# Optimization experiments

Measured on AMD Instinct MI355X. Metric: run time of the kernel, lower is better.

The kernel has to match this reference:

```python
import jax, jax.numpy as jnp
import numpy as np

B, S, H = 4, 2048, 1024
DECAY_RATE = 0.5  # MemoryModule decay: exp(-decay_rate * k), k=1 (most recent pattern)


def setup_inputs() -> dict:
    key = jax.random.key(0)
    ks = jax.random.split(key, 7)
    hidden_states = jax.random.normal(ks[0], (B, S, H), dtype=jnp.float32)
    # past attention pattern: valid row-stochastic attention probs [B, S, S]
    pa = jax.random.uniform(ks[1], (B, S, S), dtype=jnp.float32)
    past_attention = pa / pa.sum(-1, keepdims=True)
    scale = 1.0 / np.sqrt(H).astype(np.float32)
    Wq = jax.random.normal(ks[2], (H, H), dtype=jnp.float32) * scale
    Wk = jax.random.normal(ks[3], (H, H), dtype=jnp.float32) * scale
    Wv = jax.random.normal(ks[4], (H, H), dtype=jnp.float32) * scale
    Wm = jax.random.normal(ks[5], (H, H), dtype=jnp.float32) * scale
    w_gate = jax.random.normal(ks[6], (H,), dtype=jnp.float32) * scale
    return {"hidden_states": hidden_states, "past_attention": past_attention,
            "Wq": Wq, "Wk": Wk, "Wv": Wv, "Wm": Wm, "w_gate": w_gate}


def reference(hidden_states, past_attention, Wq, Wk, Wv, Wm, w_gate):
    h = hidden_states.shape[-1]
    inv_sqrt_h = 1.0 / (h ** 0.5)
    # QKV projections (hidden -> hidden)
    q = jnp.einsum('bsh,hd->bsd', hidden_states, Wq)
    k = jnp.einsum('bsh,hd->bsd', hidden_states, Wk)
    v = jnp.einsum('bsh,hd->bsd', hidden_states, Wv)
    # base attention scores QK^T / sqrt(H)
    scores = jnp.einsum('bqd,bkd->bqk', q, k) * inv_sqrt_h
    # --- memory bias ---
    # decayed history pattern (single most-recent entry, k=1)
    memory = past_attention * jnp.exp(jnp.float32(-DECAY_RATE * 1.0))  # [B,S,S]
    # per-token scalar gate from query
    gates = jax.nn.sigmoid(jnp.einsum('bsh,h->bs', q, w_gate))  # [B,S]
    memory_values = jnp.einsum('bqk,bkd->bqd', memory, v)        # memory @ V
    transformed = jnp.einsum('bsh,hd->bsd', memory_values, Wm)   # memory_transform (no bias)
    gated_memory = gates[..., None] * transformed
    memory_bias = jnp.einsum('bqd,bkd->bqk', gated_memory, k) * inv_sqrt_h
    # augmented attention
    probs = jax.nn.softmax(scores + memory_bias, axis=-1)
    context = jnp.einsum('bqk,bkd->bqd', probs, v)
    return context
```

## Files before the change

kernel.cpp:

```cpp
#include <hip/hip_runtime.h>
#include <hip/hip_bf16.h>

typedef __attribute__((ext_vector_type(4))) float f32x4;
typedef __attribute__((ext_vector_type(8))) __bf16 bf16x8;

__device__ __forceinline__ unsigned short f2bf(float f) {
    union { float f; unsigned u; } x; x.f = f;
    unsigned r = x.u + 0x7fffu + ((x.u >> 16) & 1u);
    return (unsigned short)(r >> 16);
}
__device__ __forceinline__ float bf2f(unsigned short b) {
    union { unsigned u; float f; } x; x.u = ((unsigned)b) << 16;
    return x.f;
}

__device__ __forceinline__ void gload16(const void* g, void* l) {
    __builtin_amdgcn_global_load_lds(
        (const __attribute__((address_space(1))) unsigned int*)g,
        (__attribute__((address_space(3))) unsigned int*)l,
        16, 0, 0);
}

template <int N> __device__ __forceinline__ void vm_wait();
template <> __device__ __forceinline__ void vm_wait<0>() { asm volatile("s_waitcnt vmcnt(0)" ::: "memory"); }
template <> __device__ __forceinline__ void vm_wait<2>() { asm volatile("s_waitcnt vmcnt(2)" ::: "memory"); }
template <> __device__ __forceinline__ void vm_wait<4>() { asm volatile("s_waitcnt vmcnt(4)" ::: "memory"); }

__global__ void k_convert_scale(const float* __restrict__ in, unsigned short* __restrict__ out,
                                int n4, float scale) {
    int i = blockIdx.x * 256 + threadIdx.x;
    if (i >= n4) return;
    float4 v = reinterpret_cast<const float4*>(in)[i];
    union { unsigned short u[4]; uint2 q; } o;
    o.u[0] = f2bf(v.x * scale);
    o.u[1] = f2bf(v.y * scale);
    o.u[2] = f2bf(v.z * scale);
    o.u[3] = f2bf(v.w * scale);
    reinterpret_cast<uint2*>(out)[i] = o.q;
}

__global__ void k_transpose_w(const float* __restrict__ W0, const float* __restrict__ W1,
                              const float* __restrict__ W2, const float* __restrict__ W3,
                              unsigned short* __restrict__ out) {
    __shared__ float tile[32][33];
    const float* src = blockIdx.z == 0 ? W0 : blockIdx.z == 1 ? W1 : blockIdx.z == 2 ? W2 : W3;
    unsigned short* dst = out + (size_t)blockIdx.z * 1024 * 1024;
    int lx = threadIdx.x & 31, ly8 = threadIdx.x >> 5;
    int x = blockIdx.x * 32 + lx;
#pragma unroll
    for (int i = 0; i < 4; i++) {
        int ly = ly8 + i * 8;
        tile[ly][lx] = src[(size_t)(blockIdx.y * 32 + ly) * 1024 + x];
    }
    __syncthreads();
    int tx = blockIdx.y * 32 + lx;
#pragma unroll
    for (int i = 0; i < 4; i++) {
        int ty = ly8 + i * 8;
        dst[(size_t)(blockIdx.x * 32 + ty) * 1024 + tx] = f2bf(tile[lx][ty]);
    }
}

__global__ void k_transpose_v(const unsigned short* __restrict__ C3, unsigned short* __restrict__ out) {
    __shared__ unsigned short tile[32][33];
    int bz = blockIdx.z;
    int lx = threadIdx.x & 31, ly8 = threadIdx.x >> 5;
    int x = blockIdx.x * 32 + lx;
#pragma unroll
    for (int i = 0; i < 4; i++) {
        int y = blockIdx.y * 32 + ly8 + i * 8;
        tile[ly8 + i * 8][lx] = C3[(size_t)(bz * 2048 + y) * 3072 + 2048 + x];
    }
    __syncthreads();
    int tx = blockIdx.y * 32 + lx;
#pragma unroll
    for (int i = 0; i < 4; i++) {
        int ty = blockIdx.x * 32 + ly8 + i * 8;
        out[(size_t)bz * 1024 * 2048 + (size_t)ty * 2048 + tx] = tile[lx][ly8 + i * 8];
    }
}

__global__ void k_rowdot(const float* __restrict__ A, const float* __restrict__ x,
                         float* __restrict__ out, int ncols, int sig) {
    int lane = threadIdx.x & 63;
    int row = blockIdx.x * 4 + (threadIdx.x >> 6);
    const float4* a = reinterpret_cast<const float4*>(A + (size_t)row * ncols);
    const float4* xv = reinterpret_cast<const float4*>(x);
    float s = 0.f;
    int n4 = ncols >> 2;
    for (int i = lane; i < n4; i += 64) {
        float4 av = a[i], bv = xv[i];
        s += av.x * bv.x + av.y * bv.y + av.z * bv.z + av.w * bv.w;
    }
#pragma unroll
    for (int o = 1; o < 64; o <<= 1) s += __shfl_xor(s, o);
    if (lane == 0) out[row] = sig ? (1.f / (1.f + __expf(-s))) : s;
}

__global__ __launch_bounds__(256) void k_softmax(const float* __restrict__ logits,
                                                 unsigned short* __restrict__ probs) {
    __shared__ float red[8];
    size_t base = (size_t)blockIdx.x * 2048;
    const float4* src = reinterpret_cast<const float4*>(logits + base);
    int t = threadIdx.x;
    int wave = t >> 6, lane = t & 63;
    float4 v0 = src[t], v1 = src[t + 256];
    float m = fmaxf(fmaxf(fmaxf(v0.x, v0.y), fmaxf(v0.z, v0.w)),
                    fmaxf(fmaxf(v1.x, v1.y), fmaxf(v1.z, v1.w)));
#pragma unroll
    for (int o = 1; o < 64; o <<= 1) m = fmaxf(m, __shfl_xor(m, o));
    if (lane == 0) red[wave] = m;
    __syncthreads();
    m = fmaxf(fmaxf(red[0], red[1]), fmaxf(red[2], red[3]));
    float e[8];
    e[0] = __expf(v0.x - m); e[1] = __expf(v0.y - m);
    e[2] = __expf(v0.z - m); e[3] = __expf(v0.w - m);
    e[4] = __expf(v1.x - m); e[5] = __expf(v1.y - m);
    e[6] = __expf(v1.z - m); e[7] = __expf(v1.w - m);
    float s = e[0] + e[1] + e[2] + e[3] + e[4] + e[5] + e[6] + e[7];
#pragma unroll
    for (int o = 1; o < 64; o <<= 1) s += __shfl_xor(s, o);
    if (lane == 0) red[4 + wave] = s;
    __syncthreads();
    s = red[4] + red[5] + red[6] + red[7];
    float inv = 1.f / s;
    union { unsigned short u[4]; uint2 q; } o0, o1;
#pragma unroll
    for (int j = 0; j < 4; j++) o0.u[j] = f2bf(e[j] * inv);
#pragma unroll
    for (int j = 0; j < 4; j++) o1.u[j] = f2bf(e[4 + j] * inv);
    reinterpret_cast<uint2*>(probs + base)[t] = o0.q;
    reinterpret_cast<uint2*>(probs + base)[t + 256] = o1.q;
}

template <int BN>
struct Geo {
    static constexpr int WN = BN / 64;
    static constexpr int WM = 8 / WN;
    static constexpr int WROWS = 256 / WM;
    static constexpr int MF = WROWS / 16;
    static constexpr int MP = MF / 4;
    static constexpr int ASZ = 256 * 64 * 2;
    static constexpr int BSZ = BN * 64 * 2;
    static constexpr int BUFSZ = ASZ + BSZ;
};

#define GPH(BUFOFF, MB, LB, STG, VMW)                                                   \
    {                                                                                   \
        const char* aB = smem + (BUFOFF);                                               \
        const char* bB = aB + G::ASZ;                                                   \
        bf16x8 af[G::MP * 2];                                                           \
        _Pragma("unroll") for (int mm = 0; mm < G::MP; ++mm)                            \
        _Pragma("unroll") for (int kk = 0; kk < 2; ++kk) {                              \
            int rowx = wrow + ((MB) + mm) * 16 + fr;                                    \
            int slot = (kk * 4 + kq) ^ (rowx & 7);                                      \
            af[mm * 2 + kk] = *reinterpret_cast<const bf16x8*>(aB + rowx * 128 + slot * 16); \
        }                                                                               \
        if (LB) {                                                                       \
            _Pragma("unroll") for (int nn = 0; nn < 4; ++nn)                            \
            _Pragma("unroll") for (int kk = 0; kk < 2; ++kk) {                          \
                int rowx = wcol + nn * 16 + fr;                                         \
                int slot = (kk * 4 + kq) ^ (rowx & 7);                                  \
                bfrag[nn * 2 + kk] = *reinterpret_cast<const bf16x8*>(bB + rowx * 128 + slot * 16); \
            }                                                                           \
        }                                                                               \
        STG;                                                                            \
        __builtin_amdgcn_sched_barrier(0);                                              \
        VMW;                                                                            \
        __builtin_amdgcn_s_barrier();                                                   \
        asm volatile("s_waitcnt lgkmcnt(0)" ::: "memory");                              \
        __builtin_amdgcn_sched_barrier(0);                                              \
        __builtin_amdgcn_s_setprio(1);                                                  \
        _Pragma("unroll") for (int mm = 0; mm < G::MP; ++mm)                            \
        _Pragma("unroll") for (int nn = 0; nn < 4; ++nn)                                \
        _Pragma("unroll") for (int kk = 0; kk < 2; ++kk)                                \
            acc[(MB) + mm][nn] = __builtin_amdgcn_mfma_f32_16x16x32_bf16(               \
                af[mm * 2 + kk], bfrag[nn * 2 + kk], acc[(MB) + mm][nn], 0, 0, 0);      \
        __builtin_amdgcn_s_setprio(0);                                                  \
        __builtin_amdgcn_sched_barrier(0);                                              \
        __builtin_amdgcn_s_barrier();                                                   \
        __builtin_amdgcn_sched_barrier(0);                                              \
    }

template <int EPI, int BN>
__global__ __launch_bounds__(512, 2) void k_gemm8(
    const unsigned short* __restrict__ A, int ldA, long long bsA,
    const unsigned short* __restrict__ Bt, int ldB, long long bsB,
    void* __restrict__ Cv, int ldC, long long bsC,
    const unsigned short* __restrict__ Qm, int ldQ,
    const float* __restrict__ gates, float alpha, int K, int NX, int NY) {
    using G = Geo<BN>;
    extern __shared__ char smem[];
    const int NT = K >> 6, NI = K >> 7;

    unsigned b = blockIdx.x;
    unsigned wg = (b & 7) * (gridDim.x >> 3) + (b >> 3);
    int xT = wg % NX;
    unsigned r2 = wg / NX;
    int yT = r2 % NY;
    int zB = r2 / NY;

    const unsigned short* Ab = A + (size_t)zB * (size_t)bsA;
    const unsigned short* Bb = Bt + (size_t)zB * (size_t)bsB;

    int t = threadIdx.x, lane = t & 63, wave = t >> 6;
    int wc = wave % G::WN, wr = wave / G::WN;
    int fr = lane & 15, kq = lane >> 4;
    int wrow = wr * G::WROWS, wcol = wc * 64;
    int trow = t >> 3, csx = (t & 7) ^ (trow & 7);
    long long rowTile = (long long)yT * 256, colTile = (long long)xT * BN;

    f32x4 acc[G::MF][4];
#pragma unroll
    for (int m = 0; m < G::MF; ++m)
#pragma unroll
        for (int n = 0; n < 4; ++n) acc[m][n] = (f32x4){0.f, 0.f, 0.f, 0.f};
    bf16x8 bfrag[8];

    auto stageA = [&](int buf, int h, int tt) {
        int kt = tt < NT ? tt : NT - 1;
#pragma unroll
        for (int rr = 0; rr < 2; ++rr) {
            const unsigned short* src =
                Ab + (size_t)(rowTile + h * 128 + rr * 64 + trow) * (size_t)ldA + kt * 64 + csx * 8;
            gload16(src, smem + buf * G::BUFSZ + h * 16384 + rr * 8192 + t * 16);
        }
    };
    auto stageB = [&](int buf, int h, int tt) {
        int kt = tt < NT ? tt : NT - 1;
        if (BN == 256) {
#pragma unroll
            for (int rr = 0; rr < 2; ++rr) {
                const unsigned short* src =
                    Bb + (size_t)(colTile + h * 128 + rr * 64 + trow) * (size_t)ldB + kt * 64 + csx * 8;
                gload16(src, smem + buf * G::BUFSZ + G::ASZ + h * 16384 + rr * 8192 + t * 16);
            }
        } else {
            const unsigned short* src =
                Bb + (size_t)(colTile + h * 64 + trow) * (size_t)ldB + kt * 64 + csx * 8;
            gload16(src, smem + buf * G::BUFSZ + G::ASZ + h * 8192 + t * 16);
        }
    };

    stageA(0, 0, 0); stageA(0, 1, 0);
    stageB(0, 0, 0); stageB(0, 1, 0);
    stageB(1, 0, 1); stageB(1, 1, 1);
    __builtin_amdgcn_sched_barrier(0);
    vm_wait<0>();
    __builtin_amdgcn_s_barrier();
    __builtin_amdgcn_sched_barrier(0);

    constexpr int VMN = (BN == 256) ? 4 : 2;
    for (int i = 0; i < NI; ++i) {
        int t1 = 2 * i + 1, t2 = 2 * i + 2, t3 = 2 * i + 3;
        GPH(0,          0,         1, stageA(1, 0, t1), (void)0);
        GPH(0,          G::MP,     0, stageA(1, 1, t1), (void)0);
        GPH(0,          2 * G::MP, 0, stageB(0, 0, t2), (void)0);
        GPH(0,          3 * G::MP, 0, stageB(0, 1, t2), vm_wait<VMN>());
        GPH(G::BUFSZ,   0,         1, stageA(0, 0, t2), (void)0);
        GPH(G::BUFSZ,   G::MP,     0, stageA(0, 1, t2), (void)0);
        GPH(G::BUFSZ,   2 * G::MP, 0, stageB(1, 0, t3), (void)0);
        GPH(G::BUFSZ,   3 * G::MP, 0, stageB(1, 1, t3), vm_wait<VMN>());
    }
    vm_wait<0>();

    long long rb0 = rowTile + wrow + kq * 4;
    long long cb0 = colTile + wcol + fr;
    if (EPI == 0) {
        unsigned short* C = (unsigned short*)Cv + (size_t)zB * (size_t)bsC;
#pragma unroll
        for (int m = 0; m < G::MF; ++m)
#pragma unroll
            for (int n = 0; n < 4; ++n)
#pragma unroll
                for (int r = 0; r < 4; ++r)
                    C[(size_t)(rb0 + m * 16 + r) * (size_t)ldC + cb0 + n * 16] =
                        f2bf(acc[m][n][r] * alpha);
    } else if (EPI == 1) {
        unsigned short* C = (unsigned short*)Cv;
#pragma unroll
        for (int m = 0; m < G::MF; ++m)
#pragma unroll
            for (int r = 0; r < 4; ++r) {
                long long row = rb0 + m * 16 + r;
                float g = gates[row];
#pragma unroll
                for (int n = 0; n < 4; ++n) {
                    long long col = cb0 + n * 16;
                    float v = (bf2f(Qm[(size_t)row * (size_t)ldQ + col]) + g * acc[m][n][r]) * alpha;
                    C[(size_t)row * (size_t)ldC + col] = f2bf(v);
                }
            }
    } else {
        float* C = (float*)Cv + (size_t)zB * (size_t)bsC;
#pragma unroll
        for (int m = 0; m < G::MF; ++m)
#pragma unroll
            for (int n = 0; n < 4; ++n)
#pragma unroll
                for (int r = 0; r < 4; ++r)
                    C[(size_t)(rb0 + m * 16 + r) * (size_t)ldC + cb0 + n * 16] =
                        acc[m][n][r] * alpha;
    }
}

extern "C" void kernel_launch(void* const* d_in, const int* in_sizes, int n_in,
                              void* d_out, int out_size, void* d_ws, size_t ws_size,
                              hipStream_t stream) {
    const float* hs = (const float*)d_in[0];
    const float* pa = (const float*)d_in[1];
    const float* Wq = (const float*)d_in[2];
    const float* Wk = (const float*)d_in[3];
    const float* Wv = (const float*)d_in[4];
    const float* Wm = (const float*)d_in[5];
    const float* wg = (const float*)d_in[6];
    float* out = (float*)d_out;

    const int B = 4, S = 2048, H = 1024;
    const size_t BS = (size_t)B * S;
    const size_t BSH = BS * H;
    const size_t BSS = (size_t)B * S * S;
    const float inv_sqrt_h = 0.03125f;
    const float decay = 0.60653065971263342f;

    char* ws = (char*)d_ws;
    size_t off = 0;
    auto take = [&](size_t bytes) {
        char* p = ws + off;
        off += (bytes + 255) & ~(size_t)255;
        return p;
    };
    unsigned short* hs_bf = (unsigned short*)take(BSH * 2);
    unsigned short* WT    = (unsigned short*)take(4ull * H * H * 2);
    float* wg2            = (float*)take(H * 4);
    float* gates          = (float*)take(BS * 4);
    unsigned short* C3    = (unsigned short*)take(BS * 3 * H * 2);
    unsigned short* v_t   = (unsigned short*)take(BSH * 2);
    unsigned short* pa_bf = (unsigned short*)take(BSS * 2);
    float* logits         = (float*)take(BSS * 4);
    unsigned short* mv    = (unsigned short*)d_out;
    unsigned short* u_bf  = hs_bf;
    unsigned short* probs = pa_bf;
    unsigned short* WmT   = WT + 3ull * H * H;

    (void)hipFuncSetAttribute((const void*)k_gemm8<0, 128>, hipFuncAttributeMaxDynamicSharedMemorySize, 98304);
    (void)hipFuncSetAttribute((const void*)k_gemm8<1, 128>, hipFuncAttributeMaxDynamicSharedMemorySize, 98304);
    (void)hipFuncSetAttribute((const void*)k_gemm8<2, 128>, hipFuncAttributeMaxDynamicSharedMemorySize, 98304);
    (void)hipFuncSetAttribute((const void*)k_gemm8<2, 256>, hipFuncAttributeMaxDynamicSharedMemorySize, 131072);

    k_convert_scale<<<dim3((unsigned)(BSH / 4 / 256)), 256, 0, stream>>>(hs, hs_bf, (int)(BSH / 4), 1.0f);
    k_convert_scale<<<dim3((unsigned)(BSS / 4 / 256)), 256, 0, stream>>>(pa, pa_bf, (int)(BSS / 4), decay);
    k_transpose_w<<<dim3(32, 32, 4), 256, 0, stream>>>(Wq, Wk, Wv, Wm, WT);
    k_rowdot<<<dim3(H / 4), 256, 0, stream>>>(Wq, wg, wg2, H, 0);
    k_rowdot<<<dim3((unsigned)(BS / 4)), 256, 0, stream>>>(hs, wg2, gates, H, 1);

    k_gemm8<0, 128><<<768, 512, 98304, stream>>>(
        hs_bf, H, 0, WT, H, 0, C3, 3 * H, 0, nullptr, 0, nullptr, 1.f, H, 24, 32);
    k_transpose_v<<<dim3(32, 64, 4), 256, 0, stream>>>(C3, v_t);
    k_gemm8<0, 128><<<256, 512, 98304, stream>>>(
        pa_bf, S, (long long)S * S, v_t, S, (long long)H * S, mv, H, (long long)S * H,
        nullptr, 0, nullptr, 1.f, S, 8, 8);
    k_gemm8<1, 128><<<256, 512, 98304, stream>>>(
        mv, H, 0, WmT, H, 0, u_bf, H, 0, C3, 3 * H, gates, inv_sqrt_h, H, 8, 32);
    k_gemm8<2, 256><<<256, 512, 131072, stream>>>(
        u_bf, H, (long long)S * H, C3 + H, 3 * H, (long long)S * 3 * H,
        logits, S, (long long)S * S, nullptr, 0, nullptr, 1.f, H, 8, 8);
    k_softmax<<<dim3((unsigned)BS), 256, 0, stream>>>(logits, probs);
    k_gemm8<2, 128><<<256, 512, 98304, stream>>>(
        probs, S, (long long)S * S, v_t, S, (long long)H * S, out, H, (long long)S * H,
        nullptr, 0, nullptr, 1.f, S, 8, 8);
}
```

Baseline: 274.9 us.

## Use split-K with 256-wide tiles for the S-length GEMMs, plus a reduction pass

The two K=S batched GEMMs (memory@V and probs@V) now use BN=256 tiles with a split-K of 2. Each writes fp32 partial sums into the logits scratch, and a new elementwise kernel adds the two partials and converts to bf16 or fp32. The QKV projection moves to 256-wide tiles with half the blocks. The goal is larger tiles with more data reuse while keeping 256 blocks in the grid. The cost is extra fp32 partial traffic, two additional kernel launches, and a changed fp32 summation order.

```diff
diff --git a/kernel.cpp b/kernel.cpp
--- a/kernel.cpp
+++ b/kernel.cpp
@@ -37,6 +37,30 @@
     o.u[2] = f2bf(v.z * scale);
     o.u[3] = f2bf(v.w * scale);
     reinterpret_cast<uint2*>(out)[i] = o.q;
+}
+
+__global__ void k_reduce2_bf(const float* __restrict__ p0, const float* __restrict__ p1,
+                             unsigned short* __restrict__ out, int n4) {
+    int i = blockIdx.x * 256 + threadIdx.x;
+    if (i >= n4) return;
+    float4 a = reinterpret_cast<const float4*>(p0)[i];
+    float4 b = reinterpret_cast<const float4*>(p1)[i];
+    union { unsigned short u[4]; uint2 q; } o;
+    o.u[0] = f2bf(a.x + b.x);
+    o.u[1] = f2bf(a.y + b.y);
+    o.u[2] = f2bf(a.z + b.z);
+    o.u[3] = f2bf(a.w + b.w);
+    reinterpret_cast<uint2*>(out)[i] = o.q;
+}
+__global__ void k_reduce2_f32(const float* __restrict__ p0, const float* __restrict__ p1,
+                              float* __restrict__ out, int n4) {
+    int i = blockIdx.x * 256 + threadIdx.x;
+    if (i >= n4) return;
+    float4 a = reinterpret_cast<const float4*>(p0)[i];
+    float4 b = reinterpret_cast<const float4*>(p1)[i];
+    float4 o;
+    o.x = a.x + b.x; o.y = a.y + b.y; o.z = a.z + b.z; o.w = a.w + b.w;
+    reinterpret_cast<float4*>(out)[i] = o;
 }
 
 __global__ void k_transpose_w(const float* __restrict__ W0, const float* __restrict__ W1,
@@ -188,7 +212,8 @@
     const unsigned short* __restrict__ Bt, int ldB, long long bsB,
     void* __restrict__ Cv, int ldC, long long bsC,
     const unsigned short* __restrict__ Qm, int ldQ,
-    const float* __restrict__ gates, float alpha, int K, int NX, int NY) {
+    const float* __restrict__ gates, float alpha, int K,
+    int NX, int NY, int NB, int NC) {
     using G = Geo<BN>;
     extern __shared__ char smem[];
     const int NT = K >> 6, NI = K >> 7;
@@ -198,10 +223,13 @@
     int xT = wg % NX;
     unsigned r2 = wg / NX;
     int yT = r2 % NY;
-    int zB = r2 / NY;
-
-    const unsigned short* Ab = A + (size_t)zB * (size_t)bsA;
-    const unsigned short* Bb = Bt + (size_t)zB * (size_t)bsB;
+    unsigned r3 = r2 / NY;
+    int zB = r3 % NB;
+    int c = r3 / NB;
+    int zC = c * NB + zB;
+
+    const unsigned short* Ab = A + (size_t)zB * (size_t)bsA + (size_t)c * (size_t)K;
+    const unsigned short* Bb = Bt + (size_t)zB * (size_t)bsB + (size_t)c * (size_t)K;
 
     int t = threadIdx.x, lane = t & 63, wave = t >> 6;
     int wc = wave % G::WN, wr = wave / G::WN;
@@ -267,7 +295,7 @@
     long long rb0 = rowTile + wrow + kq * 4;
     long long cb0 = colTile + wcol + fr;
     if (EPI == 0) {
-        unsigned short* C = (unsigned short*)Cv + (size_t)zB * (size_t)bsC;
+        unsigned short* C = (unsigned short*)Cv + (size_t)zC * (size_t)bsC;
 #pragma unroll
         for (int m = 0; m < G::MF; ++m)
 #pragma unroll
@@ -292,7 +320,7 @@
                 }
             }
     } else {
-        float* C = (float*)Cv + (size_t)zB * (size_t)bsC;
+        float* C = (float*)Cv + (size_t)zC * (size_t)bsC;
 #pragma unroll
         for (int m = 0; m < G::MF; ++m)
 #pragma unroll
@@ -342,10 +370,11 @@
     unsigned short* u_bf  = hs_bf;
     unsigned short* probs = pa_bf;
     unsigned short* WmT   = WT + 3ull * H * H;
-
-    (void)hipFuncSetAttribute((const void*)k_gemm8<0, 128>, hipFuncAttributeMaxDynamicSharedMemorySize, 98304);
+    float* part0 = logits;
+    float* part1 = logits + BSH;
+
+    (void)hipFuncSetAttribute((const void*)k_gemm8<0, 256>, hipFuncAttributeMaxDynamicSharedMemorySize, 131072);
     (void)hipFuncSetAttribute((const void*)k_gemm8<1, 128>, hipFuncAttributeMaxDynamicSharedMemorySize, 98304);
-    (void)hipFuncSetAttribute((const void*)k_gemm8<2, 128>, hipFuncAttributeMaxDynamicSharedMemorySize, 98304);
     (void)hipFuncSetAttribute((const void*)k_gemm8<2, 256>, hipFuncAttributeMaxDynamicSharedMemorySize, 131072);
 
     k_convert_scale<<<dim3((unsigned)(BSH / 4 / 256)), 256, 0, stream>>>(hs, hs_bf, (int)(BSH / 4), 1.0f);
@@ -354,19 +383,21 @@
     k_rowdot<<<dim3(H / 4), 256, 0, stream>>>(Wq, wg, wg2, H, 0);
     k_rowdot<<<dim3((unsigned)(BS / 4)), 256, 0, stream>>>(hs, wg2, gates, H, 1);
 
-    k_gemm8<0, 128><<<768, 512, 98304, stream>>>(
-        hs_bf, H, 0, WT, H, 0, C3, 3 * H, 0, nullptr, 0, nullptr, 1.f, H, 24, 32);
+    k_gemm8<0, 256><<<384, 512, 131072, stream>>>(
+        hs_bf, H, 0, WT, H, 0, C3, 3 * H, 0, nullptr, 0, nullptr, 1.f, H, 12, 32, 1, 1);
     k_transpose_v<<<dim3(32, 64, 4), 256, 0, stream>>>(C3, v_t);
-    k_gemm8<0, 128><<<256, 512, 98304, stream>>>(
-        pa_bf, S, (long long)S * S, v_t, S, (long long)H * S, mv, H, (long long)S * H,
-        nullptr, 0, nullptr, 1.f, S, 8, 8);
+    k_gemm8<2, 256><<<256, 512, 131072, stream>>>(
+        pa_bf, S, (long long)S * S, v_t, S, (long long)H * S, part0, H, (long long)S * H,
+        nullptr, 0, nullptr, 1.f, S / 2, 4, 8, 4, 2);
+    k_reduce2_bf<<<dim3((unsigned)(BSH / 4 / 256)), 256, 0, stream>>>(part0, part1, mv, (int)(BSH / 4));
     k_gemm8<1, 128><<<256, 512, 98304, stream>>>(
-        mv, H, 0, WmT, H, 0, u_bf, H, 0, C3, 3 * H, gates, inv_sqrt_h, H, 8, 32);
+        mv, H, 0, WmT, H, 0, u_bf, H, 0, C3, 3 * H, gates, inv_sqrt_h, H, 8, 32, 1, 1);
     k_gemm8<2, 256><<<256, 512, 131072, stream>>>(
         u_bf, H, (long long)S * H, C3 + H, 3 * H, (long long)S * 3 * H,
-        logits, S, (long long)S * S, nullptr, 0, nullptr, 1.f, H, 8, 8);
+        logits, S, (long long)S * S, nullptr, 0, nullptr, 1.f, H, 8, 8, 4, 1);
     k_softmax<<<dim3((unsigned)BS), 256, 0, stream>>>(logits, probs);
-    k_gemm8<2, 128><<<256, 512, 98304, stream>>>(
-        probs, S, (long long)S * S, v_t, S, (long long)H * S, out, H, (long long)S * H,
-        nullptr, 0, nullptr, 1.f, S, 8, 8);
-}
+    k_gemm8<2, 256><<<256, 512, 131072, stream>>>(
+        probs, S, (long long)S * S, v_t, S, (long long)H * S, part0, H, (long long)S * H,
+        nullptr, 0, nullptr, 1.f, S / 2, 4, 8, 4, 2);
+    k_reduce2_f32<<<dim3((unsigned)(BSH / 4 / 256)), 256, 0, stream>>>(part0, part1, out, (int)(BSH / 4));
+}
```

Result: slower. 304.8 us (+10.9%).

## Fuse prep and post kernels, compute gates from bf16 Q, reorder GEMM tile mapping

Applied to the files above, without the earlier changes.

Merges the conversion of hidden states, the conversion of past attention and the weight transposes into one launch. It also merges the V transpose with the gate computation, which now dots the bf16 Q already held in C3 with w_gate instead of precomputing Wq·w_gate and a separate fp32 row-dot over hidden states. It further adds a y-fastest block-to-tile mapping option for the batched GEMMs to improve L2 reuse of the B operand. This cuts launch count and removes a pass over fp32 hidden states, at the cost of slightly lower gate precision because Q is bf16.

```diff
diff --git a/kernel.cpp b/kernel.cpp
--- a/kernel.cpp
+++ b/kernel.cpp
@@ -26,75 +26,89 @@
 template <> __device__ __forceinline__ void vm_wait<2>() { asm volatile("s_waitcnt vmcnt(2)" ::: "memory"); }
 template <> __device__ __forceinline__ void vm_wait<4>() { asm volatile("s_waitcnt vmcnt(4)" ::: "memory"); }
 
-__global__ void k_convert_scale(const float* __restrict__ in, unsigned short* __restrict__ out,
-                                int n4, float scale) {
-    int i = blockIdx.x * 256 + threadIdx.x;
-    if (i >= n4) return;
-    float4 v = reinterpret_cast<const float4*>(in)[i];
-    union { unsigned short u[4]; uint2 q; } o;
-    o.u[0] = f2bf(v.x * scale);
-    o.u[1] = f2bf(v.y * scale);
-    o.u[2] = f2bf(v.z * scale);
-    o.u[3] = f2bf(v.w * scale);
-    reinterpret_cast<uint2*>(out)[i] = o.q;
-}
-
-__global__ void k_transpose_w(const float* __restrict__ W0, const float* __restrict__ W1,
-                              const float* __restrict__ W2, const float* __restrict__ W3,
-                              unsigned short* __restrict__ out) {
+__global__ __launch_bounds__(256) void k_prep(
+    const float* __restrict__ hs, const float* __restrict__ pa,
+    const float* __restrict__ Wq, const float* __restrict__ Wk,
+    const float* __restrict__ Wv, const float* __restrict__ Wm,
+    unsigned short* __restrict__ hs_bf, unsigned short* __restrict__ pa_bf,
+    unsigned short* __restrict__ WT, float decay) {
     __shared__ float tile[32][33];
-    const float* src = blockIdx.z == 0 ? W0 : blockIdx.z == 1 ? W1 : blockIdx.z == 2 ? W2 : W3;
-    unsigned short* dst = out + (size_t)blockIdx.z * 1024 * 1024;
-    int lx = threadIdx.x & 31, ly8 = threadIdx.x >> 5;
-    int x = blockIdx.x * 32 + lx;
-#pragma unroll
-    for (int i = 0; i < 4; i++) {
-        int ly = ly8 + i * 8;
-        tile[ly][lx] = src[(size_t)(blockIdx.y * 32 + ly) * 1024 + x];
-    }
-    __syncthreads();
-    int tx = blockIdx.y * 32 + lx;
-#pragma unroll
-    for (int i = 0; i < 4; i++) {
-        int ty = ly8 + i * 8;
-        dst[(size_t)(blockIdx.x * 32 + ty) * 1024 + tx] = f2bf(tile[lx][ty]);
-    }
-}
-
-__global__ void k_transpose_v(const unsigned short* __restrict__ C3, unsigned short* __restrict__ out) {
+    unsigned b = blockIdx.x;
+    int t = threadIdx.x;
+    if (b < 16384u) {
+        int i = b * 256 + t;
+        float4 v = reinterpret_cast<const float4*>(pa)[i];
+        union { unsigned short u[4]; uint2 q; } o;
+        o.u[0] = f2bf(v.x * decay); o.u[1] = f2bf(v.y * decay);
+        o.u[2] = f2bf(v.z * decay); o.u[3] = f2bf(v.w * decay);
+        reinterpret_cast<uint2*>(pa_bf)[i] = o.q;
+    } else if (b < 24576u) {
+        int i = (b - 16384u) * 256 + t;
+        float4 v = reinterpret_cast<const float4*>(hs)[i];
+        union { unsigned short u[4]; uint2 q; } o;
+        o.u[0] = f2bf(v.x); o.u[1] = f2bf(v.y);
+        o.u[2] = f2bf(v.z); o.u[3] = f2bf(v.w);
+        reinterpret_cast<uint2*>(hs_bf)[i] = o.q;
+    } else {
+        unsigned bb = b - 24576u;
+        int z = bb >> 10, rem = bb & 1023;
+        int bx = rem & 31, by = rem >> 5;
+        const float* src = z == 0 ? Wq : z == 1 ? Wk : z == 2 ? Wv : Wm;
+        unsigned short* dst = WT + (size_t)z * 1024 * 1024;
+        int lx = t & 31, ly8 = t >> 5;
+        int x = bx * 32 + lx;
+#pragma unroll
+        for (int i = 0; i < 4; i++)
+            tile[ly8 + i * 8][lx] = src[(size_t)(by * 32 + ly8 + i * 8) * 1024 + x];
+        __syncthreads();
+        int tx = by * 32 + lx;
+#pragma unroll
+        for (int i = 0; i < 4; i++)
+            dst[(size_t)(bx * 32 + ly8 + i * 8) * 1024 + tx] = f2bf(tile[lx][ly8 + i * 8]);
+    }
+}
+
+__global__ __launch_bounds__(256) void k_post(
+    const unsigned short* __restrict__ C3, unsigned short* __restrict__ v_t,
+    const float* __restrict__ wg, float* __restrict__ gates) {
     __shared__ unsigned short tile[32][33];
-    int bz = blockIdx.z;
-    int lx = threadIdx.x & 31, ly8 = threadIdx.x >> 5;
-    int x = blockIdx.x * 32 + lx;
-#pragma unroll
-    for (int i = 0; i < 4; i++) {
-        int y = blockIdx.y * 32 + ly8 + i * 8;
-        tile[ly8 + i * 8][lx] = C3[(size_t)(bz * 2048 + y) * 3072 + 2048 + x];
-    }
-    __syncthreads();
-    int tx = blockIdx.y * 32 + lx;
-#pragma unroll
-    for (int i = 0; i < 4; i++) {
-        int ty = blockIdx.x * 32 + ly8 + i * 8;
-        out[(size_t)bz * 1024 * 2048 + (size_t)ty * 2048 + tx] = tile[lx][ly8 + i * 8];
-    }
-}
-
-__global__ void k_rowdot(const float* __restrict__ A, const float* __restrict__ x,
-                         float* __restrict__ out, int ncols, int sig) {
-    int lane = threadIdx.x & 63;
-    int row = blockIdx.x * 4 + (threadIdx.x >> 6);
-    const float4* a = reinterpret_cast<const float4*>(A + (size_t)row * ncols);
-    const float4* xv = reinterpret_cast<const float4*>(x);
-    float s = 0.f;
-    int n4 = ncols >> 2;
-    for (int i = lane; i < n4; i += 64) {
-        float4 av = a[i], bv = xv[i];
-        s += av.x * bv.x + av.y * bv.y + av.z * bv.z + av.w * bv.w;
-    }
-#pragma unroll
-    for (int o = 1; o < 64; o <<= 1) s += __shfl_xor(s, o);
-    if (lane == 0) out[row] = sig ? (1.f / (1.f + __expf(-s))) : s;
+    unsigned b = blockIdx.x;
+    int t = threadIdx.x;
+    if (b < 8192u) {
+        int bx = b & 31, by = (b >> 5) & 63, bz = b >> 11;
+        int lx = t & 31, ly8 = t >> 5;
+        int x = bx * 32 + lx;
+#pragma unroll
+        for (int i = 0; i < 4; i++) {
+            int y = by * 32 + ly8 + i * 8;
+            tile[ly8 + i * 8][lx] = C3[(size_t)(bz * 2048 + y) * 3072 + 2048 + x];
+        }
+        __syncthreads();
+        int tx = by * 32 + lx;
+#pragma unroll
+        for (int i = 0; i < 4; i++) {
+            int ty = bx * 32 + ly8 + i * 8;
+            v_t[(size_t)bz * 1024 * 2048 + (size_t)ty * 2048 + tx] = tile[lx][ly8 + i * 8];
+        }
+    } else {
+        unsigned bb = b - 8192u;
+        int lane = t & 63;
+        int row = bb * 4 + (t >> 6);
+        const unsigned short* qr = C3 + (size_t)row * 3072 + lane * 16;
+        uint4 a0 = *reinterpret_cast<const uint4*>(qr);
+        uint4 a1 = *reinterpret_cast<const uint4*>(qr + 8);
+        const float* wp = wg + lane * 16;
+        float s = 0.f;
+        unsigned ua[8] = {a0.x, a0.y, a0.z, a0.w, a1.x, a1.y, a1.z, a1.w};
+#pragma unroll
+        for (int j = 0; j < 8; j++) {
+            s += bf2f((unsigned short)(ua[j] & 0xffff)) * wp[2 * j];
+            s += bf2f((unsigned short)(ua[j] >> 16)) * wp[2 * j + 1];
+        }
+#pragma unroll
+        for (int o = 1; o < 64; o <<= 1) s += __shfl_xor(s, o);
+        if (lane == 0) gates[row] = 1.f / (1.f + __expf(-s));
+    }
 }
 
 __global__ __launch_bounds__(256) void k_softmax(const float* __restrict__ logits,
@@ -188,17 +202,22 @@
     const unsigned short* __restrict__ Bt, int ldB, long long bsB,
     void* __restrict__ Cv, int ldC, long long bsC,
     const unsigned short* __restrict__ Qm, int ldQ,
-    const float* __restrict__ gates, float alpha, int K, int NX, int NY) {
+    const float* __restrict__ gates, float alpha, int K,
+    int NX, int NY, int NB, int yf) {
     using G = Geo<BN>;
     extern __shared__ char smem[];
     const int NT = K >> 6, NI = K >> 7;
 
     unsigned b = blockIdx.x;
     unsigned wg = (b & 7) * (gridDim.x >> 3) + (b >> 3);
-    int xT = wg % NX;
-    unsigned r2 = wg / NX;
-    int yT = r2 % NY;
-    int zB = r2 / NY;
+    int xT, yT, zB;
+    if (yf) {
+        yT = wg % NY; unsigned r2 = wg / NY;
+        xT = r2 % NX; zB = (int)(r2 / NX) % NB;
+    } else {
+        xT = wg % NX; unsigned r2 = wg / NX;
+        yT = r2 % NY; zB = (int)(r2 / NY) % NB;
+    }
 
     const unsigned short* Ab = A + (size_t)zB * (size_t)bsA;
     const unsigned short* Bb = Bt + (size_t)zB * (size_t)bsB;
@@ -332,7 +351,6 @@
     };
     unsigned short* hs_bf = (unsigned short*)take(BSH * 2);
     unsigned short* WT    = (unsigned short*)take(4ull * H * H * 2);
-    float* wg2            = (float*)take(H * 4);
     float* gates          = (float*)take(BS * 4);
     unsigned short* C3    = (unsigned short*)take(BS * 3 * H * 2);
     unsigned short* v_t   = (unsigned short*)take(BSH * 2);
@@ -348,25 +366,20 @@
     (void)hipFuncSetAttribute((const void*)k_gemm8<2, 128>, hipFuncAttributeMaxDynamicSharedMemorySize, 98304);
     (void)hipFuncSetAttribute((const void*)k_gemm8<2, 256>, hipFuncAttributeMaxDynamicSharedMemorySize, 131072);
 
-    k_convert_scale<<<dim3((unsigned)(BSH / 4 / 256)), 256, 0, stream>>>(hs, hs_bf, (int)(BSH / 4), 1.0f);
-    k_convert_scale<<<dim3((unsigned)(BSS / 4 / 256)), 256, 0, stream>>>(pa, pa_bf, (int)(BSS / 4), decay);
-    k_transpose_w<<<dim3(32, 32, 4), 256, 0, stream>>>(Wq, Wk, Wv, Wm, WT);
-    k_rowdot<<<dim3(H / 4), 256, 0, stream>>>(Wq, wg, wg2, H, 0);
-    k_rowdot<<<dim3((unsigned)(BS / 4)), 256, 0, stream>>>(hs, wg2, gates, H, 1);
-
+    k_prep<<<dim3(28672), 256, 0, stream>>>(hs, pa, Wq, Wk, Wv, Wm, hs_bf, pa_bf, WT, decay);
     k_gemm8<0, 128><<<768, 512, 98304, stream>>>(
-        hs_bf, H, 0, WT, H, 0, C3, 3 * H, 0, nullptr, 0, nullptr, 1.f, H, 24, 32);
-    k_transpose_v<<<dim3(32, 64, 4), 256, 0, stream>>>(C3, v_t);
+        hs_bf, H, 0, WT, H, 0, C3, 3 * H, 0, nullptr, 0, nullptr, 1.f, H, 24, 32, 1, 0);
+    k_post<<<dim3(10240), 256, 0, stream>>>(C3, v_t, wg, gates);
     k_gemm8<0, 128><<<256, 512, 98304, stream>>>(
         pa_bf, S, (long long)S * S, v_t, S, (long long)H * S, mv, H, (long long)S * H,
-        nullptr, 0, nullptr, 1.f, S, 8, 8);
+        nullptr, 0, nullptr, 1.f, S, 8, 8, 4, 1);
     k_gemm8<1, 128><<<256, 512, 98304, stream>>>(
-        mv, H, 0, WmT, H, 0, u_bf, H, 0, C3, 3 * H, gates, inv_sqrt_h, H, 8, 32);
+        mv, H, 0, WmT, H, 0, u_bf, H, 0, C3, 3 * H, gates, inv_sqrt_h, H, 8, 32, 1, 0);
     k_gemm8<2, 256><<<256, 512, 131072, stream>>>(
         u_bf, H, (long long)S * H, C3 + H, 3 * H, (long long)S * 3 * H,
-        logits, S, (long long)S * S, nullptr, 0, nullptr, 1.f, H, 8, 8);
+        logits, S, (long long)S * S, nullptr, 0, nullptr, 1.f, H, 8, 8, 4, 1);
     k_softmax<<<dim3((unsigned)BS), 256, 0, stream>>>(logits, probs);
     k_gemm8<2, 128><<<256, 512, 98304, stream>>>(
         probs, S, (long long)S * S, v_t, S, (long long)H * S, out, H, (long long)S * H,
-        nullptr, 0, nullptr, 1.f, S, 8, 8);
-}
+        nullptr, 0, nullptr, 1.f, S, 8, 8, 4, 1);
+}
```

Result: faster. 267.3 us (-2.8%).
